# Optimization experiments

Measured on AMD Instinct MI355X. Metric: run time of the kernel, lower is better.

The kernel has to match this reference:

```python
import jax, jax.numpy as jnp
import numpy as np

N_HEAD = 8  # heads; per-head scores are summed before softmax


def setup_inputs() -> dict:
    key = jax.random.key(0)
    k1, k2, k3 = jax.random.split(key, 3)
    B, T, D = 4, 512, 1024
    N, H = 16, 256  # n_concepts, init_size
    x = jax.random.normal(k1, (B, T, D), dtype=jnp.float32)
    # original init: kaiming_uniform then / d_model**2 -> very small weights; plain normal scaled similarly
    w_qs = jax.random.normal(k2, (N, D, H), dtype=jnp.float32) / (D ** 1.0)
    w_ks = jax.random.normal(k3, (N, D, H), dtype=jnp.float32) / (D ** 1.0)
    return {"x": x, "w_qs": w_qs, "w_ks": w_ks}


def reference(x, w_qs, w_ks):
    # x: [B,T,D]; w_qs/w_ks: [N,D,H]
    # Faithful to source: k_list is built from wq (source bug), so scores = q.q^T; w_ks unused in math.
    wq = jnp.einsum('btd,ndh->bnth', x, w_qs)  # [B,N,T,H]
    # Per-head split then sum over heads of q_h @ k_h^T equals the full-H contraction
    # (mask is None), so fuse: sum_h qk_h == wq @ wq^T over the whole H axis.
    attn = jnp.einsum('bnsh,bnth->bnst', wq, wq)  # temperature = 1.0; head-sum fused
    attn = jax.nn.softmax(attn, axis=-1)  # [B,N,T,T]
    # input = x.unsqueeze(1): [B,1,T,D]; einsum 'bnst,bitd->bnsd' broadcasts i=1
    e_aggregated = jnp.einsum('bnst,btd->bnsd', attn, x)  # [B,N,T,D]
    return e_aggregated, attn
```

## Files before the change

### kernel.cpp

```cpp
#include <hip/hip_runtime.h>
#include <hip/hip_bf16.h>

typedef __bf16 bf16x8 __attribute__((ext_vector_type(8)));
typedef unsigned short u16x8 __attribute__((ext_vector_type(8)));
typedef float f32x4 __attribute__((ext_vector_type(4)));
typedef __hip_bfloat16 hbf;

static constexpr int B = 4, T = 512, D = 1024, N = 16, H = 256;
static constexpr size_t E_ELEMS = (size_t)B * N * T * D;
static constexpr size_t ATTN_ELEMS = (size_t)B * N * T * T;

__device__ __forceinline__ bf16x8 load8(const hbf* p) {
  return *reinterpret_cast<const bf16x8*>(p);
}

__device__ __forceinline__ unsigned short f2bf(float f) {
  union { __hip_bfloat16 h; unsigned short u; } cv;
  cv.h = __float2bfloat16(f);
  return cv.u;
}

__device__ __forceinline__ void gload16(const hbf* g, hbf* l) {
  __builtin_amdgcn_global_load_lds(
      (const __attribute__((address_space(1))) void*)g,
      (__attribute__((address_space(3))) void*)l, 16, 0, 0);
}

template <int NWG>
__device__ __forceinline__ int xcd_swizzle(int i) {
  return (i & 7) * (NWG / 8) + (i >> 3);
}

__global__ __launch_bounds__(256) void cast_bf_k(const float* __restrict__ in,
                                                 unsigned short* __restrict__ out,
                                                 int n8) {
  int i = blockIdx.x * 256 + threadIdx.x;
  if (i >= n8) return;
  const float4* p = reinterpret_cast<const float4*>(in) + (size_t)i * 2;
  float4 a = p[0], b = p[1];
  u16x8 v;
  v[0] = f2bf(a.x); v[1] = f2bf(a.y); v[2] = f2bf(a.z); v[3] = f2bf(a.w);
  v[4] = f2bf(b.x); v[5] = f2bf(b.y); v[6] = f2bf(b.z); v[7] = f2bf(b.w);
  reinterpret_cast<u16x8*>(out)[i] = v;
}

__global__ void transpose_cast_k(const float* __restrict__ in,
                                 unsigned short* __restrict__ out, int R, int C) {
  __shared__ unsigned short tile[32][33];
  int z = blockIdx.z;
  int c0 = blockIdx.x * 32, r0 = blockIdx.y * 32;
  const float* inz = in + (size_t)z * R * C;
  unsigned short* outz = out + (size_t)z * R * C;
  int tx = threadIdx.x, ty = threadIdx.y;
  for (int i = ty; i < 32; i += 8)
    tile[i][tx] = f2bf(inz[(size_t)(r0 + i) * C + (c0 + tx)]);
  __syncthreads();
  for (int i = ty; i < 32; i += 8)
    outz[(size_t)(c0 + i) * R + (r0 + tx)] = tile[tx][i];
}

__global__ __launch_bounds__(256) void gemm_wq_tiled(const hbf* __restrict__ xb,
                                                     const hbf* __restrict__ wT,
                                                     hbf* __restrict__ wq) {
  __shared__ __align__(16) hbf As[2][128 * 32];
  __shared__ __align__(16) hbf Bs[2][64 * 32];
  int idx = xcd_swizzle<1024>(blockIdx.x);
  int b = idx >> 8, mt = (idx >> 6) & 3, jt = idx & 63;
  const hbf* A = xb + (size_t)b * T * D + (size_t)mt * 128 * D;
  const hbf* Bp = wT + (size_t)jt * 64 * D;
  int tid = threadIdx.x, wave = tid >> 6, lane = tid & 63;
  int col = lane & 15, quad = lane >> 4;
  int wm = wave & 1, wn = wave >> 1;

  auto STAGE = [&](int k0, int bi) {
    if (wave < 2) {
#pragma unroll
      for (int j = 0; j < 4; ++j) {
        int slot = (wave * 4 + j) * 64 + lane;
        int row = slot >> 2, kc = slot & 3;
        gload16(A + (size_t)row * D + k0 + kc * 8, As[bi] + slot * 8);
      }
    } else {
#pragma unroll
      for (int j = 0; j < 2; ++j) {
        int slot = ((wave - 2) * 2 + j) * 64 + lane;
        int row = slot >> 2, kc = slot & 3;
        gload16(Bp + (size_t)row * D + k0 + kc * 8, Bs[bi] + slot * 8);
      }
    }
  };

  f32x4 acc[4][2] = {};
  STAGE(0, 0);
  int cur = 0;
  for (int k0 = 0; k0 < D; k0 += 32, cur ^= 1) {
    __syncthreads();
    if (k0 + 32 < D) STAGE(k0 + 32, cur ^ 1);
    bf16x8 a[4], bb[2];
#pragma unroll
    for (int s = 0; s < 4; ++s)
      a[s] = load8(As[cur] + (wm * 64 + s * 16 + col) * 32 + quad * 8);
#pragma unroll
    for (int t = 0; t < 2; ++t)
      bb[t] = load8(Bs[cur] + (wn * 32 + t * 16 + col) * 32 + quad * 8);
#pragma unroll
    for (int s = 0; s < 4; ++s)
#pragma unroll
      for (int t = 0; t < 2; ++t)
        acc[s][t] = __builtin_amdgcn_mfma_f32_16x16x32_bf16(a[s], bb[t], acc[s][t], 0, 0, 0);
  }
  hbf* wqb = wq + (size_t)b * 16 * T * H;
#pragma unroll
  for (int s = 0; s < 4; ++s) {
    int row = mt * 128 + wm * 64 + s * 16 + quad * 4;
#pragma unroll
    for (int t = 0; t < 2; ++t) {
      int j = jt * 64 + wn * 32 + t * 16 + col;
      int n = j >> 8, h = j & 255;
      hbf* dst = wqb + (size_t)n * T * H + (size_t)row * H + h;
#pragma unroll
      for (int r = 0; r < 4; ++r)
        dst[(size_t)r * H] = __float2bfloat16(acc[s][t][r]);
    }
  }
}

__global__ __launch_bounds__(256) void attn_k(const hbf* __restrict__ wq,
                                              float* __restrict__ attn_f,
                                              hbf* __restrict__ attn_b) {
  __shared__ __align__(16) hbf Bs[2][512 * 32];
  __shared__ float redA[4][32];
  __shared__ float redB[4][32];
  int blk = xcd_swizzle<1024>(blockIdx.x);
  int bn = blk >> 4, mt = blk & 15;
  int m0 = mt * 32;
  const hbf* Wq = wq + (size_t)bn * T * H;
  int wave = threadIdx.x >> 6, lane = threadIdx.x & 63;
  int col = lane & 15, quad = lane >> 4;

  auto STAGE = [&](int k0, int bi) {
    hbf* Bl = Bs[bi];
#pragma unroll
    for (int j = 0; j < 8; ++j) {
      int slot = (wave * 8 + j) * 64 + lane;
      int row = slot >> 2, kc = slot & 3;
      gload16(Wq + (size_t)row * H + k0 + kc * 8, Bl + slot * 8);
    }
  };

  f32x4 acc[2][8] = {};
  STAGE(0, 0);
  int cur = 0;
  for (int k0 = 0; k0 < H; k0 += 32, cur ^= 1) {
    __syncthreads();
    if (k0 + 32 < H) STAGE(k0 + 32, cur ^ 1);
    bf16x8 a[2];
#pragma unroll
    for (int s = 0; s < 2; ++s)
      a[s] = load8(Bs[cur] + (m0 + s * 16 + col) * 32 + quad * 8);
#pragma unroll
    for (int t = 0; t < 8; ++t) {
      bf16x8 bfr = load8(Bs[cur] + (wave * 128 + t * 16 + col) * 32 + quad * 8);
#pragma unroll
      for (int s = 0; s < 2; ++s)
        acc[s][t] = __builtin_amdgcn_mfma_f32_16x16x32_bf16(a[s], bfr, acc[s][t], 0, 0, 0);
    }
  }

  float mrow[2][4], inv[2][4];
#pragma unroll
  for (int s = 0; s < 2; ++s)
#pragma unroll
    for (int r = 0; r < 4; ++r) {
      float pm = acc[s][0][r];
#pragma unroll
      for (int t = 1; t < 8; ++t) pm = fmaxf(pm, acc[s][t][r]);
#pragma unroll
      for (int off = 8; off >= 1; off >>= 1) pm = fmaxf(pm, __shfl_xor(pm, off));
      if (col == 0) redA[wave][s * 16 + quad * 4 + r] = pm;
    }
  __syncthreads();
#pragma unroll
  for (int s = 0; s < 2; ++s)
#pragma unroll
    for (int r = 0; r < 4; ++r) {
      int rl = s * 16 + quad * 4 + r;
      mrow[s][r] = fmaxf(fmaxf(redA[0][rl], redA[1][rl]),
                         fmaxf(redA[2][rl], redA[3][rl]));
      float sm = 0.f;
#pragma unroll
      for (int t = 0; t < 8; ++t) {
        float e = __expf(acc[s][t][r] - mrow[s][r]);
        acc[s][t][r] = e;
        sm += e;
      }
#pragma unroll
      for (int off = 8; off >= 1; off >>= 1) sm += __shfl_xor(sm, off);
      if (col == 0) redB[wave][rl] = sm;
    }
  __syncthreads();
#pragma unroll
  for (int s = 0; s < 2; ++s)
#pragma unroll
    for (int r = 0; r < 4; ++r) {
      int rl = s * 16 + quad * 4 + r;
      inv[s][r] = 1.0f / (redB[0][rl] + redB[1][rl] + redB[2][rl] + redB[3][rl]);
    }
#pragma unroll
  for (int s = 0; s < 2; ++s)
#pragma unroll
    for (int r = 0; r < 4; ++r) {
      int rl = s * 16 + quad * 4 + r;
      float iv = inv[s][r];
      size_t base = ((size_t)bn * T + m0 + rl) * T;
      float* dst = attn_f + base;
      hbf* dstb = attn_b + base;
#pragma unroll
      for (int t = 0; t < 8; ++t) {
        int c = wave * 128 + t * 16 + col;
        float p = acc[s][t][r] * iv;
        dst[c] = p;
        dstb[c] = __float2bfloat16(p);
      }
    }
}

__global__ __launch_bounds__(256) void gemm_out_tiled(const hbf* __restrict__ attn,
                                                      const hbf* __restrict__ xT,
                                                      float* __restrict__ eout) {
  __shared__ __align__(16) hbf As[2][128 * 32];
  __shared__ __align__(16) hbf Bs[2][128 * 32];
  int idx = xcd_swizzle<2048>(blockIdx.x);
  int bn = idx >> 5, mt = (idx >> 3) & 3, nt = idx & 7;
  int b = bn >> 4;
  const hbf* A = attn + (size_t)bn * T * T + (size_t)mt * 128 * T;
  const hbf* Bp = xT + (size_t)b * D * T + (size_t)nt * 128 * T;
  float* C = eout + (size_t)bn * T * D;
  int tid = threadIdx.x, wave = tid >> 6, lane = tid & 63;
  int col = lane & 15, quad = lane >> 4;
  int wm = wave & 1, wn = wave >> 1;
  const hbf* stG = (wave < 2) ? A : Bp;
  int ibase = (wave & 1) * 4;
  f32x4 acc[4][4] = {};
  {
    hbf* stL = (wave < 2) ? As[0] : Bs[0];
#pragma unroll
    for (int j = 0; j < 4; ++j) {
      int slot = (ibase + j) * 64 + lane;
      int row = slot >> 2, kc = slot & 3;
      gload16(stG + (size_t)row * T + kc * 8, stL + slot * 8);
    }
  }
  int cur = 0;
  for (int k0 = 0; k0 < T; k0 += 32, cur ^= 1) {
    __syncthreads();
    if (k0 + 32 < T) {
      hbf* stL = (wave < 2) ? As[cur ^ 1] : Bs[cur ^ 1];
#pragma unroll
      for (int j = 0; j < 4; ++j) {
        int slot = (ibase + j) * 64 + lane;
        int row = slot >> 2, kc = slot & 3;
        gload16(stG + (size_t)row * T + (k0 + 32) + kc * 8, stL + slot * 8);
      }
    }
    bf16x8 a[4], bb[4];
#pragma unroll
    for (int s = 0; s < 4; ++s)
      a[s] = load8(As[cur] + (wm * 64 + s * 16 + col) * 32 + quad * 8);
#pragma unroll
    for (int t = 0; t < 4; ++t)
      bb[t] = load8(Bs[cur] + (wn * 64 + t * 16 + col) * 32 + quad * 8);
#pragma unroll
    for (int s = 0; s < 4; ++s)
#pragma unroll
      for (int t = 0; t < 4; ++t)
        acc[s][t] = __builtin_amdgcn_mfma_f32_16x16x32_bf16(a[s], bb[t], acc[s][t], 0, 0, 0);
  }
#pragma unroll
  for (int s = 0; s < 4; ++s) {
    int row = mt * 128 + wm * 64 + s * 16 + quad * 4;
#pragma unroll
    for (int t = 0; t < 4; ++t) {
      int d = nt * 128 + wn * 64 + t * 16 + col;
      float* dst = C + (size_t)row * D + d;
#pragma unroll
      for (int r = 0; r < 4; ++r)
        dst[(size_t)r * D] = acc[s][t][r];
    }
  }
}

extern "C" void kernel_launch(void* const* d_in, const int* in_sizes, int n_in,
                              void* d_out, int out_size, void* d_ws, size_t ws_size,
                              hipStream_t stream) {
  const float* x = (const float*)d_in[0];
  const float* w_qs = (const float*)d_in[1];
  float* e_out = (float*)d_out;
  float* attn_out = e_out + E_ELEMS;

  char* ws = (char*)d_ws;
  hbf* x_bf = (hbf*)ws;
  hbf* xT   = (hbf*)(ws + (4u << 20));
  hbf* wT   = (hbf*)(ws + (8u << 20));
  hbf* wq   = (hbf*)(ws + (16u << 20));
  hbf* attn_b = (hbf*)(ws + (32u << 20));

  dim3 tb(32, 8);
  cast_bf_k<<<1024, 256, 0, stream>>>(x, (unsigned short*)x_bf, (B * T * D) / 8);
  transpose_cast_k<<<dim3(H / 32, D / 32, N), tb, 0, stream>>>(
      w_qs, (unsigned short*)wT, D, H);
  transpose_cast_k<<<dim3(D / 32, T / 32, B), tb, 0, stream>>>(
      x, (unsigned short*)xT, T, D);
  gemm_wq_tiled<<<1024, 256, 0, stream>>>(x_bf, wT, wq);
  attn_k<<<1024, 256, 0, stream>>>(wq, attn_out, attn_b);
  gemm_out_tiled<<<2048, 256, 0, stream>>>(attn_b, xT, e_out);
}
```

Measured before the change: 315.0 us.

## Rewrite output GEMM with 256x256 tiles, triple-buffered LDS and swizzled phases

```diff
diff --git a/kernel.cpp b/kernel.cpp
--- a/kernel.cpp
+++ b/kernel.cpp
@@ -225,67 +225,108 @@
     }
 }
 
-__global__ __launch_bounds__(256) void gemm_out_tiled(const hbf* __restrict__ attn,
+__global__ __launch_bounds__(512, 2) void gemm_out_8p(const hbf* __restrict__ attn,
                                                       const hbf* __restrict__ xT,
                                                       float* __restrict__ eout) {
-  __shared__ __align__(16) hbf As[2][128 * 32];
-  __shared__ __align__(16) hbf Bs[2][128 * 32];
-  int idx = xcd_swizzle<2048>(blockIdx.x);
-  int bn = idx >> 5, mt = (idx >> 3) & 3, nt = idx & 7;
+  __shared__ __align__(16) hbf Ab[3][256 * 32];
+  __shared__ __align__(16) hbf Bb[3][256 * 32];
+  int idx = xcd_swizzle<512>(blockIdx.x);
+  int bn = idx >> 3, mt = (idx >> 2) & 1, nt = idx & 3;
   int b = bn >> 4;
-  const hbf* A = attn + (size_t)bn * T * T + (size_t)mt * 128 * T;
-  const hbf* Bp = xT + (size_t)b * D * T + (size_t)nt * 128 * T;
-  float* C = eout + (size_t)bn * T * D;
-  int tid = threadIdx.x, wave = tid >> 6, lane = tid & 63;
-  int col = lane & 15, quad = lane >> 4;
-  int wm = wave & 1, wn = wave >> 1;
-  const hbf* stG = (wave < 2) ? A : Bp;
-  int ibase = (wave & 1) * 4;
-  f32x4 acc[4][4] = {};
-  {
-    hbf* stL = (wave < 2) ? As[0] : Bs[0];
+  const hbf* Ag = attn + (size_t)bn * T * T + (size_t)(mt * 256) * T;
+  const hbf* Bg = xT + (size_t)b * D * T + (size_t)(nt * 256) * T;
+  int tid = threadIdx.x;
+  int wave = tid >> 6, lane = tid & 63;
+  int c = lane & 15, quad = lane >> 4;
+  int wm = wave >> 2, wn = wave & 3;
+  int trow = tid >> 2, tks = tid & 3;
+
+  auto SWZ = [&](int row, int ks) { return row * 32 + ((ks ^ ((row >> 1) & 3)) << 3); };
+
+  auto STAGE1 = [&](int kt, int q, int bt) {
+    int half = q & 1;
+    int row = half * 128 + trow;
+    int kse = (tks ^ ((row >> 1) & 3)) << 3;
+    if (q < 2)
+      gload16(Ag + (size_t)row * T + kt * 32 + kse, Ab[bt] + half * 4096 + tid * 8);
+    else
+      gload16(Bg + (size_t)row * T + kt * 32 + kse, Bb[bt] + half * 4096 + tid * 8);
+  };
+
+  f32x4 acc[8][4] = {};
+#pragma unroll
+  for (int q = 0; q < 4; ++q) STAGE1(0, q, 0);
+#pragma unroll
+  for (int q = 0; q < 4; ++q) STAGE1(1, q, 1);
+
+  constexpr int NK = T / 32;
+  int cb = 0, st = 2;
+  bf16x8 a8[8], b4[4];
+  for (int k = 0; k < NK; ++k) {
+    bool pf = (k + 2 < NK);
+    if (k == NK - 1)
+      asm volatile("s_waitcnt vmcnt(0)" ::: "memory");
+    else
+      asm volatile("s_waitcnt vmcnt(4)" ::: "memory");
+    __builtin_amdgcn_s_barrier();
+    if (pf) STAGE1(k + 2, 0, st);
+#pragma unroll
+    for (int i = 0; i < 4; ++i) a8[i] = load8(Ab[cb] + SWZ(wm * 128 + i * 16 + c, quad));
+#pragma unroll
+    for (int j = 0; j < 2; ++j) b4[j] = load8(Bb[cb] + SWZ(wn * 64 + j * 16 + c, quad));
+    __builtin_amdgcn_s_setprio(1);
+#pragma unroll
+    for (int i = 0; i < 4; ++i)
+#pragma unroll
+      for (int j = 0; j < 2; ++j)
+        acc[i][j] = __builtin_amdgcn_mfma_f32_16x16x32_bf16(a8[i], b4[j], acc[i][j], 0, 0, 0);
+    __builtin_amdgcn_s_setprio(0);
+    __builtin_amdgcn_s_barrier();
+    if (pf) STAGE1(k + 2, 1, st);
+#pragma unroll
+    for (int i = 4; i < 8; ++i) a8[i] = load8(Ab[cb] + SWZ(wm * 128 + i * 16 + c, quad));
+    __builtin_amdgcn_s_setprio(1);
+#pragma unroll
+    for (int i = 4; i < 8; ++i)
+#pragma unroll
+      for (int j = 0; j < 2; ++j)
+        acc[i][j] = __builtin_amdgcn_mfma_f32_16x16x32_bf16(a8[i], b4[j], acc[i][j], 0, 0, 0);
+    __builtin_amdgcn_s_setprio(0);
+    __builtin_amdgcn_s_barrier();
+    if (pf) STAGE1(k + 2, 2, st);
+#pragma unroll
+    for (int j = 2; j < 4; ++j) b4[j] = load8(Bb[cb] + SWZ(wn * 64 + j * 16 + c, quad));
+    __builtin_amdgcn_s_setprio(1);
+#pragma unroll
+    for (int i = 0; i < 4; ++i)
+#pragma unroll
+      for (int j = 2; j < 4; ++j)
+        acc[i][j] = __builtin_amdgcn_mfma_f32_16x16x32_bf16(a8[i], b4[j], acc[i][j], 0, 0, 0);
+    __builtin_amdgcn_s_setprio(0);
+    __builtin_amdgcn_s_barrier();
+    if (pf) STAGE1(k + 2, 3, st);
+    __builtin_amdgcn_s_setprio(1);
+#pragma unroll
+    for (int i = 4; i < 8; ++i)
+#pragma unroll
+      for (int j = 2; j < 4; ++j)
+        acc[i][j] = __builtin_amdgcn_mfma_f32_16x16x32_bf16(a8[i], b4[j], acc[i][j], 0, 0, 0);
+    __builtin_amdgcn_s_setprio(0);
+    cb = (cb == 2) ? 0 : cb + 1;
+    st = (st == 2) ? 0 : st + 1;
+  }
+
+  float* Cc = eout + (size_t)bn * T * D;
+#pragma unroll
+  for (int i = 0; i < 8; ++i) {
+    int grow = mt * 256 + wm * 128 + i * 16 + quad * 4;
 #pragma unroll
     for (int j = 0; j < 4; ++j) {
-      int slot = (ibase + j) * 64 + lane;
-      int row = slot >> 2, kc = slot & 3;
-      gload16(stG + (size_t)row * T + kc * 8, stL + slot * 8);
-    }
-  }
-  int cur = 0;
-  for (int k0 = 0; k0 < T; k0 += 32, cur ^= 1) {
-    __syncthreads();
-    if (k0 + 32 < T) {
-      hbf* stL = (wave < 2) ? As[cur ^ 1] : Bs[cur ^ 1];
-#pragma unroll
-      for (int j = 0; j < 4; ++j) {
-        int slot = (ibase + j) * 64 + lane;
-        int row = slot >> 2, kc = slot & 3;
-        gload16(stG + (size_t)row * T + (k0 + 32) + kc * 8, stL + slot * 8);
-      }
-    }
-    bf16x8 a[4], bb[4];
-#pragma unroll
-    for (int s = 0; s < 4; ++s)
-      a[s] = load8(As[cur] + (wm * 64 + s * 16 + col) * 32 + quad * 8);
-#pragma unroll
-    for (int t = 0; t < 4; ++t)
-      bb[t] = load8(Bs[cur] + (wn * 64 + t * 16 + col) * 32 + quad * 8);
-#pragma unroll
-    for (int s = 0; s < 4; ++s)
-#pragma unroll
-      for (int t = 0; t < 4; ++t)
-        acc[s][t] = __builtin_amdgcn_mfma_f32_16x16x32_bf16(a[s], bb[t], acc[s][t], 0, 0, 0);
-  }
-#pragma unroll
-  for (int s = 0; s < 4; ++s) {
-    int row = mt * 128 + wm * 64 + s * 16 + quad * 4;
-#pragma unroll
-    for (int t = 0; t < 4; ++t) {
-      int d = nt * 128 + wn * 64 + t * 16 + col;
-      float* dst = C + (size_t)row * D + d;
+      int gcol = nt * 256 + wn * 64 + j * 16 + c;
+      float* dst = Cc + (size_t)grow * D + gcol;
 #pragma unroll
       for (int r = 0; r < 4; ++r)
-        dst[(size_t)r * D] = acc[s][t][r];
+        dst[(size_t)r * D] = acc[i][j][r];
     }
   }
 }
@@ -313,5 +354,5 @@
       x, (unsigned short*)xT, T, D);
   gemm_wq_tiled<<<1024, 256, 0, stream>>>(x_bf, wT, wq);
   attn_k<<<1024, 256, 0, stream>>>(wq, attn_out, attn_b);
-  gemm_out_tiled<<<2048, 256, 0, stream>>>(attn_b, xT, e_out);
-}
+  gemm_out_8p<<<512, 512, 0, stream>>>(attn_b, xT, e_out);
+}
```

After: 330.3 us. 4.9% more time.
